# Kernel optimization log

Hardware: AMD Instinct MI355X
Metric: run time of the kernel (lower is better)

Reference implementation:

```python
import jax, jax.numpy as jnp
import numpy as np

# Detectron-style RPN GenerateProposals config (cfg[...].RPN_* in the original)
PRE_NMS_TOP_N = 6000
POST_NMS_TOP_N = 1000
NMS_THRESH = 0.7
MIN_SIZE = 16.0
FEAT_STRIDE = 16.0  # 1 / spatial_scale
BBOX_XFORM_CLIP = float(np.log(1000.0 / 16.0))


def _make_anchors():
    # 5 scales x 3 aspect ratios, centered at origin (Detectron-style)
    sizes = [32.0, 64.0, 128.0, 256.0, 512.0]
    ratios = [0.5, 1.0, 2.0]
    out = []
    for s in sizes:
        for r in ratios:
            w = s * np.sqrt(1.0 / r)
            h = s * np.sqrt(r)
            out.append([-(w - 1) / 2.0, -(h - 1) / 2.0, (w - 1) / 2.0, (h - 1) / 2.0])
    return np.asarray(out, dtype=np.float32)  # (15, 4)


def setup_inputs() -> dict:
    key = jax.random.key(0)
    k1, k2 = jax.random.split(key)
    N, A, H, W = 2, 15, 200, 200
    rpn_cls_prob = jax.random.uniform(k1, (N, A, H, W), dtype=jnp.float32)
    rpn_bbox_pred = jax.random.normal(k2, (N, 4 * A, H, W), dtype=jnp.float32) * 0.1
    im_h = H * FEAT_STRIDE
    im_w = W * FEAT_STRIDE
    im_info = jnp.tile(jnp.array([[im_h, im_w, 1.0]], dtype=jnp.float32), (N, 1))
    anchors = jnp.asarray(_make_anchors())
    return {"rpn_cls_prob": rpn_cls_prob, "rpn_bbox_pred": rpn_bbox_pred,
            "im_info": im_info, "anchors": anchors}


def _decode(anchors, deltas):
    # box_utils.bbox_transform with weights (1,1,1,1)
    ws = anchors[:, 2] - anchors[:, 0] + 1.0
    hs = anchors[:, 3] - anchors[:, 1] + 1.0
    cx = anchors[:, 0] + 0.5 * ws
    cy = anchors[:, 1] + 0.5 * hs
    dx, dy = deltas[:, 0], deltas[:, 1]
    dw = jnp.minimum(deltas[:, 2], BBOX_XFORM_CLIP)
    dh = jnp.minimum(deltas[:, 3], BBOX_XFORM_CLIP)
    pcx = dx * ws + cx
    pcy = dy * hs + cy
    pw = jnp.exp(dw) * ws
    ph = jnp.exp(dh) * hs
    return jnp.stack([pcx - 0.5 * pw, pcy - 0.5 * ph,
                      pcx + 0.5 * pw - 1.0, pcy + 0.5 * ph - 1.0], axis=1)


def _iou_matrix(boxes):
    # (P,4) -> (P,P), with +1 convention matching the original numpy code
    x1, y1, x2, y2 = boxes[:, 0], boxes[:, 1], boxes[:, 2], boxes[:, 3]
    areas = (x2 - x1 + 1.0) * (y2 - y1 + 1.0)
    xx1 = jnp.maximum(x1[:, None], x1[None, :])
    yy1 = jnp.maximum(y1[:, None], y1[None, :])
    xx2 = jnp.minimum(x2[:, None], x2[None, :])
    yy2 = jnp.minimum(y2[:, None], y2[None, :])
    iw = jnp.maximum(xx2 - xx1 + 1.0, 0.0)
    ih = jnp.maximum(yy2 - yy1 + 1.0, 0.0)
    inter = iw * ih
    return inter / (areas[:, None] + areas[None, :] - inter)


def _proposals_one_image(scores, deltas, im_info_i, all_anchors):
    # scores: (A,H,W); deltas: (4A,H,W); all_anchors: (K*A,4)
    P = PRE_NMS_TOP_N
    s = scores.transpose(1, 2, 0).reshape(-1)          # (K*A,)
    d = deltas.transpose(1, 2, 0).reshape(-1, 4)       # (K*A,4)
    vals, idx = jax.lax.top_k(s, P)                    # pre-NMS top-k
    props = _decode(all_anchors[idx], d[idx])          # (P,4)
    im_h, im_w, im_scale = im_info_i[0], im_info_i[1], im_info_i[2]
    # clip_tiled_boxes
    x1 = jnp.clip(props[:, 0], 0.0, im_w - 1.0)
    y1 = jnp.clip(props[:, 1], 0.0, im_h - 1.0)
    x2 = jnp.clip(props[:, 2], 0.0, im_w - 1.0)
    y2 = jnp.clip(props[:, 3], 0.0, im_h - 1.0)
    props = jnp.stack([x1, y1, x2, y2], axis=1)
    # _filter_boxes: mask out instead of removing (static shapes)
    min_size = MIN_SIZE * im_scale
    ws = x2 - x1 + 1.0
    hs = y2 - y1 + 1.0
    xc = x1 + ws / 2.0
    yc = y1 + hs / 2.0
    valid = (ws >= min_size) & (hs >= min_size) & (xc < im_w) & (yc < im_h)
    sc = jnp.where(valid, vals, -jnp.inf)
    order = jnp.argsort(-sc)                           # valid boxes first, by score
    props = props[order]
    sc = sc[order]
    valid = valid[order]
    # greedy NMS on score-sorted boxes
    iou = jax.lax.stop_gradient(_iou_matrix(props))    # (P,P)
    pos = jnp.arange(P)

    def step(keep, i):
        sup = (iou[i] > NMS_THRESH) & (pos > i) & keep[i]
        return keep & ~sup, None

    keep, _ = jax.lax.scan(step, valid, jnp.arange(P))
    final_sc = jnp.where(keep, sc, -jnp.inf)
    top_vals, top_idx = jax.lax.top_k(final_sc, POST_NMS_TOP_N)
    ok = jnp.isfinite(top_vals)
    out_props = jnp.where(ok[:, None], props[top_idx], 0.0)
    out_sc = jnp.where(ok, top_vals, 0.0)
    return out_props, out_sc


def reference(rpn_cls_prob, rpn_bbox_pred, im_info, anchors):
    N, A, H, W = rpn_cls_prob.shape
    # anchor shifting: all_anchors (K*A, 4)
    shift_x = jnp.arange(W, dtype=jnp.float32) * FEAT_STRIDE
    shift_y = jnp.arange(H, dtype=jnp.float32) * FEAT_STRIDE
    sx, sy = jnp.meshgrid(shift_x, shift_y)            # 'xy', matches np.meshgrid
    shifts = jnp.stack([sx.ravel(), sy.ravel(), sx.ravel(), sy.ravel()], axis=1)
    all_anchors = (anchors[None, :, :] + shifts[:, None, :]).reshape(-1, 4)
    props, sc = jax.vmap(
        lambda s, d, ii: _proposals_one_image(s, d, ii, all_anchors)
    )(rpn_cls_prob, rpn_bbox_pred, im_info)            # (N,R,4), (N,R)
    R = POST_NMS_TOP_N
    batch_inds = jnp.broadcast_to(
        jnp.arange(N, dtype=jnp.float32)[:, None, None], (N, R, 1))
    rois = jnp.concatenate([batch_inds, props], axis=2).reshape(N * R, 5)
    roi_probs = sc.reshape(N * R, 1)
    # pack [batch_ind, x1, y1, x2, y2, score] into one fixed-shape array
    return jnp.concatenate([rois, roi_probs], axis=1)  # (N*R, 6)
```

## Files before the change

kernel.cpp:

```cpp
#include <hip/hip_runtime.h>
#include <stdint.h>

#define N_IMG 2
#define A_NUM 15
#define HH 200
#define WW 200
#define HW 40000
#define K_TOT 600000
#define K_TOT4 150000
#define P_PRE 6000
#define R_POST 1000
#define NMS_T 0.7f
#define MIN_SZ 16.0f
#define FSTRIDE 16.0f
#define BBOX_CLIP 4.135166556742356f
#define CAND_CAP 8192
#define NWORDS 94
#define BINS 4096
#define MASK_BLOCKS 600
#define ZERO_WORDS (N_IMG * BINS * 2 + N_IMG * 16)
#define MID_T 0.7000000178813934326171875

typedef unsigned long long u64;
typedef uint32_t u32;

__device__ __forceinline__ u32 fkey(float s) {
    return __float_as_uint(s) | 0x80000000u;
}

__device__ __forceinline__ bool iou_gt(float ar, float arj,
                                       const float4& bi, const float4& bj) {
    float xx1 = fmaxf(bi.x, bj.x);
    float yy1 = fmaxf(bi.y, bj.y);
    float xx2 = fminf(bi.z, bj.z);
    float yy2 = fminf(bi.w, bj.w);
    float iw = fmaxf(xx2 - xx1 + 1.0f, 0.0f);
    float ih = fmaxf(yy2 - yy1 + 1.0f, 0.0f);
    float inter = iw * ih;
    float uni = (ar + arj) - inter;
    return (double)inter >= MID_T * (double)uni;
}

__global__ void k_zero(u32* __restrict__ w) {
    int i = blockIdx.x * 1024 + threadIdx.x;
    if (i < ZERO_WORDS) w[i] = 0u;
}

__global__ void k_histA(const float* __restrict__ sc, u32* __restrict__ histA,
                        u32* __restrict__ meta) {
    int n = blockIdx.y;
    __shared__ u32 h[BINS];
    __shared__ u32 part[256];
    __shared__ u32 isLast;
    for (int i = threadIdx.x; i < BINS; i += 256) h[i] = 0;
    __syncthreads();
    const float4* s4 = (const float4*)(sc + (size_t)n * K_TOT);
    for (int i = blockIdx.x * 256 + threadIdx.x; i < K_TOT4; i += 64 * 256) {
        float4 v = s4[i];
        atomicAdd(&h[fkey(v.x) >> 20], 1u);
        atomicAdd(&h[fkey(v.y) >> 20], 1u);
        atomicAdd(&h[fkey(v.z) >> 20], 1u);
        atomicAdd(&h[fkey(v.w) >> 20], 1u);
    }
    __syncthreads();
    for (int i = threadIdx.x; i < BINS; i += 256) {
        u32 v = h[i];
        if (v) atomicAdd(&histA[n * BINS + i], v);
    }
    __threadfence();
    if (threadIdx.x == 0)
        isLast = (atomicAdd(&meta[6], 1u) == (u32)(64 * N_IMG - 1)) ? 1u : 0u;
    __syncthreads();
    if (!isLast) return;
    for (int im = 0; im < N_IMG; ++im) {
        u32* hh = histA + im * BINS;
        u32 s = 0;
        for (int b = threadIdx.x * 16; b < threadIdx.x * 16 + 16; ++b)
            s += atomicAdd(&hh[b], 0u);
        part[threadIdx.x] = s;
        __syncthreads();
        if (threadIdx.x == 0) {
            u32 cum = 0; int seg = 255;
            for (; seg > 0; --seg) {
                if (cum + part[seg] >= P_PRE) break;
                cum += part[seg];
            }
            u32 cgt = cum; int bA = seg * 16; u32 hbA = 0;
            for (int b = seg * 16 + 15; b >= seg * 16; --b) {
                u32 hb = atomicAdd(&hh[b], 0u);
                if (cgt + hb >= P_PRE) { bA = b; hbA = hb; break; }
                cgt += hb;
            }
            meta[im * 16 + 0] = (u32)bA;
            meta[im * 16 + 1] = cgt;
            if (cgt + hbA <= CAND_CAP) {
                meta[im * 16 + 2] = ((u32)bA) << 12;
                meta[im * 16 + 8] = 0u;
            } else {
                meta[im * 16 + 8] = 1u;
            }
        }
        __syncthreads();
    }
}

__global__ void k_histB(const float* __restrict__ sc, u32* __restrict__ histB,
                        u32* __restrict__ meta) {
    int n = blockIdx.y;
    if (meta[n * 16 + 8] == 0u) return;
    __shared__ u32 h[BINS];
    __shared__ u32 part[256];
    __shared__ u32 isLast;
    for (int i = threadIdx.x; i < BINS; i += 256) h[i] = 0;
    __syncthreads();
    u32 bA = meta[n * 16 + 0];
    const float4* s4 = (const float4*)(sc + (size_t)n * K_TOT);
    for (int i = blockIdx.x * 256 + threadIdx.x; i < K_TOT4; i += 64 * 256) {
        float4 v = s4[i];
        u32 k0 = fkey(v.x), k1 = fkey(v.y), k2 = fkey(v.z), k3 = fkey(v.w);
        if ((k0 >> 20) == bA) atomicAdd(&h[(k0 >> 8) & 0xFFFu], 1u);
        if ((k1 >> 20) == bA) atomicAdd(&h[(k1 >> 8) & 0xFFFu], 1u);
        if ((k2 >> 20) == bA) atomicAdd(&h[(k2 >> 8) & 0xFFFu], 1u);
        if ((k3 >> 20) == bA) atomicAdd(&h[(k3 >> 8) & 0xFFFu], 1u);
    }
    __syncthreads();
    for (int i = threadIdx.x; i < BINS; i += 256) {
        u32 v = h[i];
        if (v) atomicAdd(&histB[n * BINS + i], v);
    }
    __threadfence();
    if (threadIdx.x == 0)
        isLast = (atomicAdd(&meta[n * 16 + 7], 1u) == 63u) ? 1u : 0u;
    __syncthreads();
    if (!isLast) return;
    {
        int im = n;
        u32* hh = histB + im * BINS;
        u32 s = 0;
        for (int b = threadIdx.x * 16; b < threadIdx.x * 16 + 16; ++b)
            s += atomicAdd(&hh[b], 0u);
        part[threadIdx.x] = s;
        __syncthreads();
        if (threadIdx.x == 0) {
            u32 cum = meta[im * 16 + 1];
            int seg = 255;
            for (; seg > 0; --seg) {
                if (cum + part[seg] >= P_PRE) break;
                cum += part[seg];
            }
            int bB = seg * 16;
            for (int b = seg * 16 + 15; b >= seg * 16; --b) {
                u32 hb = atomicAdd(&hh[b], 0u);
                if (cum + hb >= P_PRE) { bB = b; break; }
                cum += hb;
            }
            meta[im * 16 + 2] = (meta[im * 16 + 0] << 12) | (u32)bB;
        }
    }
}

__global__ void __launch_bounds__(256) k_compact(const float* __restrict__ sc,
                                                 u32* __restrict__ meta,
                                                 u64* __restrict__ cand) {
    int n = blockIdx.y;
    int tid = threadIdx.x;
    int lane = tid & 63, w = tid >> 6;
    int i4 = blockIdx.x * 256 + tid;
    u32 thr = meta[n * 16 + 2];
    float vv[4] = {0.f, 0.f, 0.f, 0.f};
    u32 flags = 0;
    if (i4 < K_TOT4) {
        const float4* s4 = (const float4*)(sc + (size_t)n * K_TOT);
        float4 v = s4[i4];
        vv[0] = v.x; vv[1] = v.y; vv[2] = v.z; vv[3] = v.w;
        #pragma unroll
        for (int e = 0; e < 4; ++e)
            if ((fkey(vv[e]) >> 8) >= thr) flags |= 1u << e;
    }
    u32 cnt = (u32)__popc(flags);
    u32 incl = cnt;
    #pragma unroll
    for (int off = 1; off < 64; off <<= 1) {
        u32 v = __shfl_up(incl, (unsigned)off);
        if (lane >= off) incl += v;
    }
    __shared__ u32 wtot[4];
    __shared__ u32 baseS;
    if (lane == 63) wtot[w] = incl;
    __syncthreads();
    if (tid == 0) {
        u32 tot = wtot[0] + wtot[1] + wtot[2] + wtot[3];
        baseS = atomicAdd(&meta[n * 16 + 3], tot);
    }
    __syncthreads();
    if (!flags) return;
    u32 wbase = 0;
    for (int i = 0; i < w; ++i) wbase += wtot[i];
    u32 pos = baseS + wbase + (incl - cnt);
    #pragma unroll
    for (int e = 0; e < 4; ++e) {
        if ((flags >> e) & 1u) {
            if (pos < CAND_CAP) {
                int el = i4 * 4 + e;
                int a = el / HW;
                int r = el - a * HW;
                u32 idx = (u32)(r * A_NUM + a);
                cand[n * CAND_CAP + pos] = ((u64)fkey(vv[e]) << 32) | (u32)(~idx);
            }
            pos++;
        }
    }
}

__global__ void __launch_bounds__(256) k_rankdec(
        const u64* __restrict__ cand, const u32* __restrict__ meta,
        const float* __restrict__ bbox, const float* __restrict__ iminfo,
        const float* __restrict__ anchors,
        float* __restrict__ topk_sc, float4* __restrict__ bbox4,
        u32* __restrict__ bval) {
    int n = blockIdx.y;
    u32 cnt = meta[n * 16 + 3];
    if (cnt > CAND_CAP) cnt = CAND_CAP;
    int base = blockIdx.x * 64;
    if (base >= (int)cnt) return;
    __shared__ u64 sk[CAND_CAP];
    __shared__ u32 pr[4][64];
    int tid = threadIdx.x, lane = tid & 63, w = tid >> 6;
    int cntPad = (int)((cnt + 7u) & ~7u);
    const u64* cn = cand + (size_t)n * CAND_CAP;
    for (int i = tid; i < cntPad; i += 256)
        sk[i] = (i < (int)cnt) ? cn[i] : 0ull;
    __syncthreads();
    int myi = base + lane;
    u64 mykey = (myi < (int)cnt) ? sk[myi] : 0ull;
    int stride = ((cntPad >> 2) + 7) & ~7;
    int j0 = w * stride;
    int j1 = min(j0 + stride, cntPad);
    int rank = 0;
    for (int j = j0; j < j1; j += 8) {
        u64 k0 = sk[j + 0], k1 = sk[j + 1], k2 = sk[j + 2], k3 = sk[j + 3];
        u64 k4 = sk[j + 4], k5 = sk[j + 5], k6 = sk[j + 6], k7 = sk[j + 7];
        rank += (int)(k0 > mykey) + (int)(k1 > mykey)
              + (int)(k2 > mykey) + (int)(k3 > mykey)
              + (int)(k4 > mykey) + (int)(k5 > mykey)
              + (int)(k6 > mykey) + (int)(k7 > mykey);
    }
    pr[w][lane] = (u32)rank;
    __syncthreads();
    if (w != 0 || myi >= (int)cnt) return;
    int r = (int)(pr[0][lane] + pr[1][lane] + pr[2][lane] + pr[3][lane]);
    if (r >= P_PRE) return;
    u32 idx = ~(u32)(mykey & 0xFFFFFFFFull);
    float score = __uint_as_float((u32)(mykey >> 32) ^ 0x80000000u);
    topk_sc[n * P_PRE + r] = score;
    int a = (int)(idx % A_NUM);
    int cell = (int)(idx / A_NUM);
    int ww = cell % WW, hh = cell / WW;
    float ax1 = anchors[a * 4 + 0] + FSTRIDE * (float)ww;
    float ay1 = anchors[a * 4 + 1] + FSTRIDE * (float)hh;
    float ax2 = anchors[a * 4 + 2] + FSTRIDE * (float)ww;
    float ay2 = anchors[a * 4 + 3] + FSTRIDE * (float)hh;
    float ws = ax2 - ax1 + 1.0f;
    float hs = ay2 - ay1 + 1.0f;
    float cx = ax1 + 0.5f * ws;
    float cy = ay1 + 0.5f * hs;
    const float* bb = bbox + (size_t)n * 4 * A_NUM * HW + hh * WW + ww;
    float dx = bb[(4 * a + 0) * HW];
    float dy = bb[(4 * a + 1) * HW];
    float dw = fminf(bb[(4 * a + 2) * HW], BBOX_CLIP);
    float dh = fminf(bb[(4 * a + 3) * HW], BBOX_CLIP);
    float pcx = dx * ws + cx, pcy = dy * hs + cy;
    float pw = expf(dw) * ws, ph = expf(dh) * hs;
    float x1 = pcx - 0.5f * pw;
    float y1 = pcy - 0.5f * ph;
    float x2 = pcx + 0.5f * pw - 1.0f;
    float y2 = pcy + 0.5f * ph - 1.0f;
    float im_h = iminfo[n * 3 + 0], im_w = iminfo[n * 3 + 1], iscale = iminfo[n * 3 + 2];
    x1 = fminf(fmaxf(x1, 0.0f), im_w - 1.0f);
    y1 = fminf(fmaxf(y1, 0.0f), im_h - 1.0f);
    x2 = fminf(fmaxf(x2, 0.0f), im_w - 1.0f);
    y2 = fminf(fmaxf(y2, 0.0f), im_h - 1.0f);
    float wss = x2 - x1 + 1.0f, hss = y2 - y1 + 1.0f;
    float xc = x1 + wss * 0.5f, yc = y1 + hss * 0.5f;
    float ms = MIN_SZ * iscale;
    bool valid = (wss >= ms) && (hss >= ms) && (xc < im_w) && (yc < im_h);
    float4 b; b.x = x1; b.y = y1; b.z = x2; b.w = y2;
    bbox4[n * P_PRE + r] = b;
    bval[n * P_PRE + r] = valid ? 1u : 0u;
}

__global__ void __launch_bounds__(1024) k_partition(
        const float4* __restrict__ bbox4,
        const float* __restrict__ bsc, const u32* __restrict__ bval,
        float4* __restrict__ sbox, float* __restrict__ ssc,
        float* __restrict__ sarea, u32* __restrict__ meta) {
    int n = blockIdx.x;
    int t = threadIdx.x;
    int lane = t & 63, w = t >> 6;
    int base = t * 6;
    u32 cnt = 0;
    if (base < P_PRE)
        for (int e = 0; e < 6; ++e) cnt += bval[n * P_PRE + base + e];
    u32 incl = cnt;
    #pragma unroll
    for (int off = 1; off < 64; off <<= 1) {
        u32 v = __shfl_up(incl, (unsigned)off);
        if (lane >= off) incl += v;
    }
    __shared__ u32 wtot[16];
    if (lane == 63) wtot[w] = incl;
    __syncthreads();
    u32 nv = 0, wbase = 0;
    #pragma unroll
    for (int i = 0; i < 16; ++i) {
        u32 x = wtot[i];
        if (i < w) wbase += x;
        nv += x;
    }
    u32 excl = wbase + (incl - cnt);
    if (t == 0) meta[n * 16 + 4] = nv;
    if (base < P_PRE) {
        u32 vseen = excl;
        for (int e = 0; e < 6; ++e) {
            int g = base + e;
            int src = n * P_PRE + g;
            u32 dst;
            if (bval[src]) { dst = vseen; vseen++; }
            else { dst = nv + (u32)g - vseen; }
            int d = n * P_PRE + (int)dst;
            float4 b = bbox4[src];
            sbox[d] = b;
            ssc[d] = bsc[src];
            sarea[d] = (b.z - b.x + 1.0f) * (b.w - b.y + 1.0f);
        }
    }
}

__global__ void __launch_bounds__(256) k_mask(const float4* __restrict__ sbox,
                                              const float* __restrict__ sarea,
                                              u64* __restrict__ mask,
                                              u64* __restrict__ selfmask) {
    int n = blockIdx.y;
    int rem = blockIdx.x;
    int ci = 0;
    while (true) {
        int g = (NWORDS - ci + 7) >> 3;
        if (rem < g) break;
        rem -= g;
        ++ci;
    }
    int cjBase = ci + (rem << 3);
    int lane = threadIdx.x & 63;
    int wv = threadIdx.x >> 6;
    __shared__ float4 sbi[64];
    __shared__ float sar[64];
    const float4* pb = sbox + n * P_PRE;
    const float* pa = sarea + n * P_PRE;
    if (threadIdx.x < 64) {
        int ic = min(ci * 64 + (int)threadIdx.x, P_PRE - 1);
        sbi[threadIdx.x] = pb[ic];
        sar[threadIdx.x] = pa[ic];
    }
    __syncthreads();
    #pragma unroll
    for (int sub = 0; sub < 2; ++sub) {
        int cj = cjBase + wv + sub * 4;
        if (cj >= NWORDS) continue;
        int j = cj * 64 + lane;
        int jc = min(j, P_PRE - 1);
        float4 bj = pb[jc];
        float arj = pa[jc];
        if (cj == ci) {
            u64 sm = 0;
            #pragma unroll 8
            for (int r = 0; r < 64; ++r) {
                bool sup = iou_gt(sar[r], arj, sbi[r], bj) && (r < lane);
                sm |= ((u64)sup) << r;
            }
            if (j < P_PRE) selfmask[(size_t)n * P_PRE + j] = sm;
        } else {
            u64 myword = 0;
            #pragma unroll 8
            for (int r = 0; r < 64; ++r) {
                u64 wrd = __ballot(iou_gt(sar[r], arj, sbi[r], bj));
                if (lane == r) myword = wrd;
            }
            int i = ci * 64 + lane;
            if (i < P_PRE)
                mask[((size_t)n * P_PRE + i) * NWORDS + cj] = myword;
        }
    }
}

__global__ void __launch_bounds__(1024) k_scan(
        const u64* __restrict__ mask, const u64* __restrict__ selfmask,
        const float4* __restrict__ sbox, const float* __restrict__ ssc,
        const u32* __restrict__ meta, float* __restrict__ out) {
    int n = blockIdx.x;
    int tid = threadIdx.x;
    int lane = tid & 63;
    int wv = tid >> 6;
    __shared__ u64 rem[NWORDS];
    __shared__ u64 smb[2][64];
    __shared__ u64 sA;
    __shared__ u32 rowsS[64];
    __shared__ int nkS;
    __shared__ u32 kidx[R_POST];
    __shared__ int keptS;
    u32 nv = meta[n * 16 + 4];
    const u64* mrow = mask + (size_t)n * P_PRE * NWORDS;
    const u64* smk = selfmask + (size_t)n * P_PRE;
    for (int c = tid; c < NWORDS; c += 1024) {
        int b0 = c * 64;
        rem[c] = ((u32)b0 >= nv) ? ~0ull
               : (((u32)(nv - b0) >= 64u) ? 0ull : ((~0ull) << (nv - b0)));
    }
    if (wv == 1) smb[0][lane] = smk[lane];
    if (tid == 0) keptS = 0;
    __syncthreads();
    for (int c = 0; c < NWORDS; ++c) {
        if (wv == 1 && (c + 1) < NWORDS) {
            int j = (c + 1) * 64 + lane;
            smb[(c + 1) & 1][lane] = (j < P_PRE) ? smk[j] : 0ull;
        }
        if (wv == 0) {
            u64 A = ~rem[c];
            if (A) {
                u64 sm = smb[c & 1][lane];
                u64 below = (1ull << lane) - 1ull;
                bool cand = ((A >> lane) & 1ull) != 0ull;
                while (true) {
                    bool sup = (sm & A & below) != 0ull;
                    u64 nA = __ballot(cand && !sup);
                    if (nA == A) break;
                    A = nA;
                }
                int kept = keptS;
                if ((A >> lane) & 1ull) {
                    int rk = (int)__popcll(A & below);
                    int pos = kept + rk;
                    if (pos < R_POST) kidx[pos] = (u32)(c * 64 + lane);
                    rowsS[rk] = (u32)lane;
                }
                if (lane == 0) {
                    keptS = kept + (int)__popcll(A);
                    nkS = (int)__popcll(A);
                    sA = A;
                }
            } else if (lane == 0) { sA = 0; nkS = 0; }
        }
        __syncthreads();
        if (keptS >= R_POST) break;
        if (sA) {
            int colSlot = tid & 127;
            int rg = tid >> 7;
            int col = c + 1 + colSlot;
            int nk = nkS;
            if (col < NWORDS && rg < nk) {
                int jbase = c * 64;
                u64 acc = 0;
                for (int r = rg; r < nk; r += 32) {
                    int r1 = r + 8, r2 = r + 16, r3 = r + 24;
                    u64 v0 = mrow[(size_t)(jbase + (int)rowsS[r]) * NWORDS + col];
                    u64 v1 = (r1 < nk) ? mrow[(size_t)(jbase + (int)rowsS[r1]) * NWORDS + col] : 0ull;
                    u64 v2 = (r2 < nk) ? mrow[(size_t)(jbase + (int)rowsS[r2]) * NWORDS + col] : 0ull;
                    u64 v3 = (r3 < nk) ? mrow[(size_t)(jbase + (int)rowsS[r3]) * NWORDS + col] : 0ull;
                    acc |= v0 | v1 | v2 | v3;
                }
                if (acc) atomicOr(&rem[col], acc);
            }
        }
        __syncthreads();
    }
    __syncthreads();
    int kept = keptS;
    for (int r = tid; r < R_POST; r += 1024) {
        float4 b = make_float4(0.f, 0.f, 0.f, 0.f);
        float s = 0.f;
        if (r < kept) {
            u32 i = kidx[r];
            b = sbox[n * P_PRE + (int)i];
            s = ssc[n * P_PRE + (int)i];
        }
        float* o = out + (size_t)(n * R_POST + r) * 6;
        o[0] = (float)n;
        o[1] = b.x; o[2] = b.y; o[3] = b.z; o[4] = b.w; o[5] = s;
    }
}

extern "C" void kernel_launch(void* const* d_in, const int* in_sizes, int n_in,
                              void* d_out, int out_size, void* d_ws, size_t ws_size,
                              hipStream_t stream) {
    const float* scores  = (const float*)d_in[0];
    const float* bbox    = (const float*)d_in[1];
    const float* iminfo  = (const float*)d_in[2];
    const float* anchors = (const float*)d_in[3];
    float* out = (float*)d_out;

    char* ws = (char*)d_ws;
    size_t off = 0;
    u32* histA = (u32*)(ws + off); off += (size_t)N_IMG * BINS * 4;
    u32* histB = (u32*)(ws + off); off += (size_t)N_IMG * BINS * 4;
    u32* meta  = (u32*)(ws + off); off += (size_t)N_IMG * 16 * 4;
    u64* cand      = (u64*)(ws + off);   off += (size_t)N_IMG * CAND_CAP * 8;
    float* topk_sc = (float*)(ws + off); off += (size_t)N_IMG * P_PRE * 4;
    float4* bbox4 = (float4*)(ws + off); off += (size_t)N_IMG * P_PRE * 16;
    u32* bval  = (u32*)(ws + off);       off += (size_t)N_IMG * P_PRE * 4;
    float4* sbox = (float4*)(ws + off);  off += (size_t)N_IMG * P_PRE * 16;
    float* ssc = (float*)(ws + off);     off += (size_t)N_IMG * P_PRE * 4;
    float* sarea = (float*)(ws + off);   off += (size_t)N_IMG * P_PRE * 4;
    u64* selfmask = (u64*)(ws + off);    off += (size_t)N_IMG * P_PRE * 8;
    u64* mask = (u64*)(ws + off);        off += (size_t)N_IMG * P_PRE * NWORDS * 8;
    (void)ws_size; (void)in_sizes; (void)n_in; (void)out_size;

    k_zero<<<(ZERO_WORDS + 1023) / 1024, 1024, 0, stream>>>((u32*)d_ws);

    dim3 gHist(64, N_IMG);
    k_histA<<<gHist, 256, 0, stream>>>(scores, histA, meta);
    k_histB<<<gHist, 256, 0, stream>>>(scores, histB, meta);
    dim3 gComp((K_TOT4 + 255) / 256, N_IMG);
    k_compact<<<gComp, 256, 0, stream>>>(scores, meta, cand);
    dim3 gRank(CAND_CAP / 64, N_IMG);
    k_rankdec<<<gRank, 256, 0, stream>>>(cand, meta, bbox, iminfo, anchors,
                                         topk_sc, bbox4, bval);
    k_partition<<<N_IMG, 1024, 0, stream>>>(bbox4, topk_sc, bval, sbox, ssc, sarea, meta);
    dim3 gMask(MASK_BLOCKS, N_IMG);
    k_mask<<<gMask, 256, 0, stream>>>(sbox, sarea, mask, selfmask);
    k_scan<<<N_IMG, 1024, 0, stream>>>(mask, selfmask, sbox, ssc, meta, out);
}
```

Baseline: 164.4 us.

## Fuse front-end top-k stages into one cooperative kernel with grid syncs

Replaces the zero, two histogram, compaction and rank/decode kernels with a single cooperative kernel of 128 blocks. Stages are separated by grid.sync instead of separate launches and last-block atomics. This removes several launch gaps. In exchange, compaction and rank/decode now run on only 128 blocks in loops instead of ~1200 and 256 blocks, which reduces parallelism.

```diff
diff --git a/kernel.cpp b/kernel.cpp
--- a/kernel.cpp
+++ b/kernel.cpp
@@ -1,5 +1,8 @@
 #include <hip/hip_runtime.h>
+#include <hip/hip_cooperative_groups.h>
 #include <stdint.h>
+
+namespace cg = cooperative_groups;
 
 #define N_IMG 2
 #define A_NUM 15
@@ -41,21 +44,35 @@
     return (double)inter >= MID_T * (double)uni;
 }
 
-__global__ void k_zero(u32* __restrict__ w) {
-    int i = blockIdx.x * 1024 + threadIdx.x;
-    if (i < ZERO_WORDS) w[i] = 0u;
-}
-
-__global__ void k_histA(const float* __restrict__ sc, u32* __restrict__ histA,
-                        u32* __restrict__ meta) {
-    int n = blockIdx.y;
-    __shared__ u32 h[BINS];
-    __shared__ u32 part[256];
-    __shared__ u32 isLast;
-    for (int i = threadIdx.x; i < BINS; i += 256) h[i] = 0;
+__global__ void __launch_bounds__(256) k_front(
+        const float* __restrict__ sc, const float* __restrict__ bbox,
+        const float* __restrict__ iminfo, const float* __restrict__ anchors,
+        u32* __restrict__ histA, u32* __restrict__ histB, u32* __restrict__ meta,
+        u64* __restrict__ cand, float* __restrict__ topk_sc,
+        float4* __restrict__ bbox4, u32* __restrict__ bval) {
+    cg::grid_group grid = cg::this_grid();
+    __shared__ u64 sk[CAND_CAP];
+    u32* h     = (u32*)sk;
+    u32* part  = (u32*)sk + BINS;
+    u32* wtot  = (u32*)sk + BINS + 256;
+    u32* baseS = (u32*)sk + BINS + 260;
+    u32* pr    = (u32*)sk + 16000;
+    int bid = blockIdx.x;
+    int tid = threadIdx.x;
+    int lane = tid & 63, w = tid >> 6;
+    int n = bid >> 6;
+    int bl = bid & 63;
+    const float4* s4 = (const float4*)(sc + (size_t)n * K_TOT);
+
+    {
+        int i = bid * 256 + tid;
+        if (i < ZERO_WORDS) histA[i] = 0u;
+    }
+    grid.sync();
+
+    for (int i = tid; i < BINS; i += 256) h[i] = 0;
     __syncthreads();
-    const float4* s4 = (const float4*)(sc + (size_t)n * K_TOT);
-    for (int i = blockIdx.x * 256 + threadIdx.x; i < K_TOT4; i += 64 * 256) {
+    for (int i = bl * 256 + tid; i < K_TOT4; i += 64 * 256) {
         float4 v = s4[i];
         atomicAdd(&h[fkey(v.x) >> 20], 1u);
         atomicAdd(&h[fkey(v.y) >> 20], 1u);
@@ -63,230 +80,222 @@
         atomicAdd(&h[fkey(v.w) >> 20], 1u);
     }
     __syncthreads();
-    for (int i = threadIdx.x; i < BINS; i += 256) {
+    for (int i = tid; i < BINS; i += 256) {
         u32 v = h[i];
         if (v) atomicAdd(&histA[n * BINS + i], v);
     }
-    __threadfence();
-    if (threadIdx.x == 0)
-        isLast = (atomicAdd(&meta[6], 1u) == (u32)(64 * N_IMG - 1)) ? 1u : 0u;
-    __syncthreads();
-    if (!isLast) return;
-    for (int im = 0; im < N_IMG; ++im) {
-        u32* hh = histA + im * BINS;
-        u32 s = 0;
-        for (int b = threadIdx.x * 16; b < threadIdx.x * 16 + 16; ++b)
-            s += atomicAdd(&hh[b], 0u);
-        part[threadIdx.x] = s;
-        __syncthreads();
-        if (threadIdx.x == 0) {
-            u32 cum = 0; int seg = 255;
-            for (; seg > 0; --seg) {
-                if (cum + part[seg] >= P_PRE) break;
-                cum += part[seg];
-            }
-            u32 cgt = cum; int bA = seg * 16; u32 hbA = 0;
-            for (int b = seg * 16 + 15; b >= seg * 16; --b) {
-                u32 hb = atomicAdd(&hh[b], 0u);
-                if (cgt + hb >= P_PRE) { bA = b; hbA = hb; break; }
-                cgt += hb;
-            }
-            meta[im * 16 + 0] = (u32)bA;
-            meta[im * 16 + 1] = cgt;
-            if (cgt + hbA <= CAND_CAP) {
-                meta[im * 16 + 2] = ((u32)bA) << 12;
-                meta[im * 16 + 8] = 0u;
-            } else {
-                meta[im * 16 + 8] = 1u;
-            }
-        }
-        __syncthreads();
-    }
-}
-
-__global__ void k_histB(const float* __restrict__ sc, u32* __restrict__ histB,
-                        u32* __restrict__ meta) {
-    int n = blockIdx.y;
-    if (meta[n * 16 + 8] == 0u) return;
-    __shared__ u32 h[BINS];
-    __shared__ u32 part[256];
-    __shared__ u32 isLast;
-    for (int i = threadIdx.x; i < BINS; i += 256) h[i] = 0;
-    __syncthreads();
-    u32 bA = meta[n * 16 + 0];
-    const float4* s4 = (const float4*)(sc + (size_t)n * K_TOT);
-    for (int i = blockIdx.x * 256 + threadIdx.x; i < K_TOT4; i += 64 * 256) {
-        float4 v = s4[i];
-        u32 k0 = fkey(v.x), k1 = fkey(v.y), k2 = fkey(v.z), k3 = fkey(v.w);
-        if ((k0 >> 20) == bA) atomicAdd(&h[(k0 >> 8) & 0xFFFu], 1u);
-        if ((k1 >> 20) == bA) atomicAdd(&h[(k1 >> 8) & 0xFFFu], 1u);
-        if ((k2 >> 20) == bA) atomicAdd(&h[(k2 >> 8) & 0xFFFu], 1u);
-        if ((k3 >> 20) == bA) atomicAdd(&h[(k3 >> 8) & 0xFFFu], 1u);
-    }
-    __syncthreads();
-    for (int i = threadIdx.x; i < BINS; i += 256) {
-        u32 v = h[i];
-        if (v) atomicAdd(&histB[n * BINS + i], v);
-    }
-    __threadfence();
-    if (threadIdx.x == 0)
-        isLast = (atomicAdd(&meta[n * 16 + 7], 1u) == 63u) ? 1u : 0u;
-    __syncthreads();
-    if (!isLast) return;
+    grid.sync();
+
+    if (bid == 0) {
+        for (int im = 0; im < N_IMG; ++im) {
+            u32* hh = histA + im * BINS;
+            u32 s = 0;
+            for (int b = tid * 16; b < tid * 16 + 16; ++b) s += hh[b];
+            part[tid] = s;
+            __syncthreads();
+            if (tid == 0) {
+                u32 cum = 0; int seg = 255;
+                for (; seg > 0; --seg) {
+                    if (cum + part[seg] >= P_PRE) break;
+                    cum += part[seg];
+                }
+                u32 cgt = cum; int bA = seg * 16; u32 hbA = 0;
+                for (int b = seg * 16 + 15; b >= seg * 16; --b) {
+                    u32 hb = hh[b];
+                    if (cgt + hb >= P_PRE) { bA = b; hbA = hb; break; }
+                    cgt += hb;
+                }
+                meta[im * 16 + 0] = (u32)bA;
+                meta[im * 16 + 1] = cgt;
+                if (cgt + hbA <= CAND_CAP) {
+                    meta[im * 16 + 2] = ((u32)bA) << 12;
+                    meta[im * 16 + 8] = 0u;
+                } else {
+                    meta[im * 16 + 8] = 1u;
+                }
+            }
+            __syncthreads();
+        }
+    }
+    grid.sync();
+
+    bool needB = (meta[8] != 0u) || (meta[16 + 8] != 0u);
+    if (needB) {
+        bool mine = meta[n * 16 + 8] != 0u;
+        for (int i = tid; i < BINS; i += 256) h[i] = 0;
+        __syncthreads();
+        if (mine) {
+            u32 bA = meta[n * 16 + 0];
+            for (int i = bl * 256 + tid; i < K_TOT4; i += 64 * 256) {
+                float4 v = s4[i];
+                u32 k0 = fkey(v.x), k1 = fkey(v.y), k2 = fkey(v.z), k3 = fkey(v.w);
+                if ((k0 >> 20) == bA) atomicAdd(&h[(k0 >> 8) & 0xFFFu], 1u);
+                if ((k1 >> 20) == bA) atomicAdd(&h[(k1 >> 8) & 0xFFFu], 1u);
+                if ((k2 >> 20) == bA) atomicAdd(&h[(k2 >> 8) & 0xFFFu], 1u);
+                if ((k3 >> 20) == bA) atomicAdd(&h[(k3 >> 8) & 0xFFFu], 1u);
+            }
+        }
+        __syncthreads();
+        if (mine)
+            for (int i = tid; i < BINS; i += 256) {
+                u32 v = h[i];
+                if (v) atomicAdd(&histB[n * BINS + i], v);
+            }
+        grid.sync();
+        if (bid == 0) {
+            for (int im = 0; im < N_IMG; ++im) {
+                if (meta[im * 16 + 8] == 0u) continue;
+                u32* hh = histB + im * BINS;
+                u32 s = 0;
+                for (int b = tid * 16; b < tid * 16 + 16; ++b) s += hh[b];
+                part[tid] = s;
+                __syncthreads();
+                if (tid == 0) {
+                    u32 cum = meta[im * 16 + 1];
+                    int seg = 255;
+                    for (; seg > 0; --seg) {
+                        if (cum + part[seg] >= P_PRE) break;
+                        cum += part[seg];
+                    }
+                    int bB = seg * 16;
+                    for (int b = seg * 16 + 15; b >= seg * 16; --b) {
+                        u32 hb = hh[b];
+                        if (cum + hb >= P_PRE) { bB = b; break; }
+                        cum += hb;
+                    }
+                    meta[im * 16 + 2] = (meta[im * 16 + 0] << 12) | (u32)bB;
+                }
+                __syncthreads();
+            }
+        }
+        grid.sync();
+    }
+
     {
-        int im = n;
-        u32* hh = histB + im * BINS;
-        u32 s = 0;
-        for (int b = threadIdx.x * 16; b < threadIdx.x * 16 + 16; ++b)
-            s += atomicAdd(&hh[b], 0u);
-        part[threadIdx.x] = s;
-        __syncthreads();
-        if (threadIdx.x == 0) {
-            u32 cum = meta[im * 16 + 1];
-            int seg = 255;
-            for (; seg > 0; --seg) {
-                if (cum + part[seg] >= P_PRE) break;
-                cum += part[seg];
-            }
-            int bB = seg * 16;
-            for (int b = seg * 16 + 15; b >= seg * 16; --b) {
-                u32 hb = atomicAdd(&hh[b], 0u);
-                if (cum + hb >= P_PRE) { bB = b; break; }
-                cum += hb;
-            }
-            meta[im * 16 + 2] = (meta[im * 16 + 0] << 12) | (u32)bB;
-        }
-    }
-}
-
-__global__ void __launch_bounds__(256) k_compact(const float* __restrict__ sc,
-                                                 u32* __restrict__ meta,
-                                                 u64* __restrict__ cand) {
-    int n = blockIdx.y;
-    int tid = threadIdx.x;
-    int lane = tid & 63, w = tid >> 6;
-    int i4 = blockIdx.x * 256 + tid;
-    u32 thr = meta[n * 16 + 2];
-    float vv[4] = {0.f, 0.f, 0.f, 0.f};
-    u32 flags = 0;
-    if (i4 < K_TOT4) {
-        const float4* s4 = (const float4*)(sc + (size_t)n * K_TOT);
-        float4 v = s4[i4];
-        vv[0] = v.x; vv[1] = v.y; vv[2] = v.z; vv[3] = v.w;
-        #pragma unroll
-        for (int e = 0; e < 4; ++e)
-            if ((fkey(vv[e]) >> 8) >= thr) flags |= 1u << e;
-    }
-    u32 cnt = (u32)__popc(flags);
-    u32 incl = cnt;
-    #pragma unroll
-    for (int off = 1; off < 64; off <<= 1) {
-        u32 v = __shfl_up(incl, (unsigned)off);
-        if (lane >= off) incl += v;
-    }
-    __shared__ u32 wtot[4];
-    __shared__ u32 baseS;
-    if (lane == 63) wtot[w] = incl;
-    __syncthreads();
-    if (tid == 0) {
-        u32 tot = wtot[0] + wtot[1] + wtot[2] + wtot[3];
-        baseS = atomicAdd(&meta[n * 16 + 3], tot);
-    }
-    __syncthreads();
-    if (!flags) return;
-    u32 wbase = 0;
-    for (int i = 0; i < w; ++i) wbase += wtot[i];
-    u32 pos = baseS + wbase + (incl - cnt);
-    #pragma unroll
-    for (int e = 0; e < 4; ++e) {
-        if ((flags >> e) & 1u) {
-            if (pos < CAND_CAP) {
-                int el = i4 * 4 + e;
-                int a = el / HW;
-                int r = el - a * HW;
-                u32 idx = (u32)(r * A_NUM + a);
-                cand[n * CAND_CAP + pos] = ((u64)fkey(vv[e]) << 32) | (u32)(~idx);
-            }
-            pos++;
-        }
-    }
-}
-
-__global__ void __launch_bounds__(256) k_rankdec(
-        const u64* __restrict__ cand, const u32* __restrict__ meta,
-        const float* __restrict__ bbox, const float* __restrict__ iminfo,
-        const float* __restrict__ anchors,
-        float* __restrict__ topk_sc, float4* __restrict__ bbox4,
-        u32* __restrict__ bval) {
-    int n = blockIdx.y;
-    u32 cnt = meta[n * 16 + 3];
-    if (cnt > CAND_CAP) cnt = CAND_CAP;
-    int base = blockIdx.x * 64;
-    if (base >= (int)cnt) return;
-    __shared__ u64 sk[CAND_CAP];
-    __shared__ u32 pr[4][64];
-    int tid = threadIdx.x, lane = tid & 63, w = tid >> 6;
-    int cntPad = (int)((cnt + 7u) & ~7u);
-    const u64* cn = cand + (size_t)n * CAND_CAP;
-    for (int i = tid; i < cntPad; i += 256)
-        sk[i] = (i < (int)cnt) ? cn[i] : 0ull;
-    __syncthreads();
-    int myi = base + lane;
-    u64 mykey = (myi < (int)cnt) ? sk[myi] : 0ull;
-    int stride = ((cntPad >> 2) + 7) & ~7;
-    int j0 = w * stride;
-    int j1 = min(j0 + stride, cntPad);
-    int rank = 0;
-    for (int j = j0; j < j1; j += 8) {
-        u64 k0 = sk[j + 0], k1 = sk[j + 1], k2 = sk[j + 2], k3 = sk[j + 3];
-        u64 k4 = sk[j + 4], k5 = sk[j + 5], k6 = sk[j + 6], k7 = sk[j + 7];
-        rank += (int)(k0 > mykey) + (int)(k1 > mykey)
-              + (int)(k2 > mykey) + (int)(k3 > mykey)
-              + (int)(k4 > mykey) + (int)(k5 > mykey)
-              + (int)(k6 > mykey) + (int)(k7 > mykey);
-    }
-    pr[w][lane] = (u32)rank;
-    __syncthreads();
-    if (w != 0 || myi >= (int)cnt) return;
-    int r = (int)(pr[0][lane] + pr[1][lane] + pr[2][lane] + pr[3][lane]);
-    if (r >= P_PRE) return;
-    u32 idx = ~(u32)(mykey & 0xFFFFFFFFull);
-    float score = __uint_as_float((u32)(mykey >> 32) ^ 0x80000000u);
-    topk_sc[n * P_PRE + r] = score;
-    int a = (int)(idx % A_NUM);
-    int cell = (int)(idx / A_NUM);
-    int ww = cell % WW, hh = cell / WW;
-    float ax1 = anchors[a * 4 + 0] + FSTRIDE * (float)ww;
-    float ay1 = anchors[a * 4 + 1] + FSTRIDE * (float)hh;
-    float ax2 = anchors[a * 4 + 2] + FSTRIDE * (float)ww;
-    float ay2 = anchors[a * 4 + 3] + FSTRIDE * (float)hh;
-    float ws = ax2 - ax1 + 1.0f;
-    float hs = ay2 - ay1 + 1.0f;
-    float cx = ax1 + 0.5f * ws;
-    float cy = ay1 + 0.5f * hs;
-    const float* bb = bbox + (size_t)n * 4 * A_NUM * HW + hh * WW + ww;
-    float dx = bb[(4 * a + 0) * HW];
-    float dy = bb[(4 * a + 1) * HW];
-    float dw = fminf(bb[(4 * a + 2) * HW], BBOX_CLIP);
-    float dh = fminf(bb[(4 * a + 3) * HW], BBOX_CLIP);
-    float pcx = dx * ws + cx, pcy = dy * hs + cy;
-    float pw = expf(dw) * ws, ph = expf(dh) * hs;
-    float x1 = pcx - 0.5f * pw;
-    float y1 = pcy - 0.5f * ph;
-    float x2 = pcx + 0.5f * pw - 1.0f;
-    float y2 = pcy + 0.5f * ph - 1.0f;
-    float im_h = iminfo[n * 3 + 0], im_w = iminfo[n * 3 + 1], iscale = iminfo[n * 3 + 2];
-    x1 = fminf(fmaxf(x1, 0.0f), im_w - 1.0f);
-    y1 = fminf(fmaxf(y1, 0.0f), im_h - 1.0f);
-    x2 = fminf(fmaxf(x2, 0.0f), im_w - 1.0f);
-    y2 = fminf(fmaxf(y2, 0.0f), im_h - 1.0f);
-    float wss = x2 - x1 + 1.0f, hss = y2 - y1 + 1.0f;
-    float xc = x1 + wss * 0.5f, yc = y1 + hss * 0.5f;
-    float ms = MIN_SZ * iscale;
-    bool valid = (wss >= ms) && (hss >= ms) && (xc < im_w) && (yc < im_h);
-    float4 b; b.x = x1; b.y = y1; b.z = x2; b.w = y2;
-    bbox4[n * P_PRE + r] = b;
-    bval[n * P_PRE + r] = valid ? 1u : 0u;
+        u32 thr = meta[n * 16 + 2];
+        const int ITERS = (K_TOT4 + 64 * 256 - 1) / (64 * 256);
+        for (int it = 0; it < ITERS; ++it) {
+            int i4 = it * (64 * 256) + bl * 256 + tid;
+            float vv[4] = {0.f, 0.f, 0.f, 0.f};
+            u32 flags = 0;
+            if (i4 < K_TOT4) {
+                float4 v = s4[i4];
+                vv[0] = v.x; vv[1] = v.y; vv[2] = v.z; vv[3] = v.w;
+                #pragma unroll
+                for (int e = 0; e < 4; ++e)
+                    if ((fkey(vv[e]) >> 8) >= thr) flags |= 1u << e;
+            }
+            u32 cnt = (u32)__popc(flags);
+            u32 incl = cnt;
+            #pragma unroll
+            for (int off = 1; off < 64; off <<= 1) {
+                u32 v = __shfl_up(incl, (unsigned)off);
+                if (lane >= off) incl += v;
+            }
+            if (lane == 63) wtot[w] = incl;
+            __syncthreads();
+            if (tid == 0) {
+                u32 tot = wtot[0] + wtot[1] + wtot[2] + wtot[3];
+                *baseS = atomicAdd(&meta[n * 16 + 3], tot);
+            }
+            __syncthreads();
+            if (flags) {
+                u32 wbase = 0;
+                for (int i = 0; i < w; ++i) wbase += wtot[i];
+                u32 pos = *baseS + wbase + (incl - cnt);
+                #pragma unroll
+                for (int e = 0; e < 4; ++e) {
+                    if ((flags >> e) & 1u) {
+                        if (pos < CAND_CAP) {
+                            int el = i4 * 4 + e;
+                            int a = el / HW;
+                            int r = el - a * HW;
+                            u32 idx = (u32)(r * A_NUM + a);
+                            cand[n * CAND_CAP + pos] = ((u64)fkey(vv[e]) << 32) | (u32)(~idx);
+                        }
+                        pos++;
+                    }
+                }
+            }
+            __syncthreads();
+        }
+    }
+    grid.sync();
+
+    for (int g = bid; g < 2 * (CAND_CAP / 64); g += 128) {
+        int n2 = g >> 7;
+        int base = (g & 127) * 64;
+        u32 cnt = meta[n2 * 16 + 3];
+        if (cnt > CAND_CAP) cnt = CAND_CAP;
+        if (base >= (int)cnt) continue;
+        int cntPad = (int)((cnt + 7u) & ~7u);
+        const u64* cn = cand + (size_t)n2 * CAND_CAP;
+        __syncthreads();
+        for (int i = tid; i < cntPad; i += 256)
+            sk[i] = (i < (int)cnt) ? cn[i] : 0ull;
+        __syncthreads();
+        int myi = base + lane;
+        u64 mykey = (myi < (int)cnt) ? sk[myi] : 0ull;
+        int stride = ((cntPad >> 2) + 7) & ~7;
+        int j0 = w * stride;
+        int j1 = min(j0 + stride, cntPad);
+        int rank = 0;
+        for (int j = j0; j < j1; j += 8) {
+            u64 k0 = sk[j + 0], k1 = sk[j + 1], k2 = sk[j + 2], k3 = sk[j + 3];
+            u64 k4 = sk[j + 4], k5 = sk[j + 5], k6 = sk[j + 6], k7 = sk[j + 7];
+            rank += (int)(k0 > mykey) + (int)(k1 > mykey)
+                  + (int)(k2 > mykey) + (int)(k3 > mykey)
+                  + (int)(k4 > mykey) + (int)(k5 > mykey)
+                  + (int)(k6 > mykey) + (int)(k7 > mykey);
+        }
+        pr[w * 64 + lane] = (u32)rank;
+        __syncthreads();
+        if (w == 0 && myi < (int)cnt) {
+            int r = (int)(pr[lane] + pr[64 + lane] + pr[128 + lane] + pr[192 + lane]);
+            if (r < P_PRE) {
+                u64 kk = mykey;
+                u32 idx = ~(u32)(kk & 0xFFFFFFFFull);
+                float score = __uint_as_float((u32)(kk >> 32) ^ 0x80000000u);
+                topk_sc[n2 * P_PRE + r] = score;
+                int a = (int)(idx % A_NUM);
+                int cell = (int)(idx / A_NUM);
+                int ww = cell % WW, hh = cell / WW;
+                float ax1 = anchors[a * 4 + 0] + FSTRIDE * (float)ww;
+                float ay1 = anchors[a * 4 + 1] + FSTRIDE * (float)hh;
+                float ax2 = anchors[a * 4 + 2] + FSTRIDE * (float)ww;
+                float ay2 = anchors[a * 4 + 3] + FSTRIDE * (float)hh;
+                float ws = ax2 - ax1 + 1.0f;
+                float hs = ay2 - ay1 + 1.0f;
+                float cx = ax1 + 0.5f * ws;
+                float cy = ay1 + 0.5f * hs;
+                const float* bb = bbox + (size_t)n2 * 4 * A_NUM * HW + hh * WW + ww;
+                float dx = bb[(4 * a + 0) * HW];
+                float dy = bb[(4 * a + 1) * HW];
+                float dw = fminf(bb[(4 * a + 2) * HW], BBOX_CLIP);
+                float dh = fminf(bb[(4 * a + 3) * HW], BBOX_CLIP);
+                float pcx = dx * ws + cx, pcy = dy * hs + cy;
+                float pw = expf(dw) * ws, ph = expf(dh) * hs;
+                float x1 = pcx - 0.5f * pw;
+                float y1 = pcy - 0.5f * ph;
+                float x2 = pcx + 0.5f * pw - 1.0f;
+                float y2 = pcy + 0.5f * ph - 1.0f;
+                float im_h = iminfo[n2 * 3 + 0], im_w = iminfo[n2 * 3 + 1];
+                float iscale = iminfo[n2 * 3 + 2];
+                x1 = fminf(fmaxf(x1, 0.0f), im_w - 1.0f);
+                y1 = fminf(fmaxf(y1, 0.0f), im_h - 1.0f);
+                x2 = fminf(fmaxf(x2, 0.0f), im_w - 1.0f);
+                y2 = fminf(fmaxf(y2, 0.0f), im_h - 1.0f);
+                float wss = x2 - x1 + 1.0f, hss = y2 - y1 + 1.0f;
+                float xc = x1 + wss * 0.5f, yc = y1 + hss * 0.5f;
+                float ms = MIN_SZ * iscale;
+                bool valid = (wss >= ms) && (hss >= ms) && (xc < im_w) && (yc < im_h);
+                float4 b; b.x = x1; b.y = y1; b.z = x2; b.w = y2;
+                bbox4[n2 * P_PRE + r] = b;
+                bval[n2 * P_PRE + r] = valid ? 1u : 0u;
+            }
+        }
+        __syncthreads();
+    }
 }
 
 __global__ void __launch_bounds__(1024) k_partition(
@@ -513,16 +522,11 @@
     u64* mask = (u64*)(ws + off);        off += (size_t)N_IMG * P_PRE * NWORDS * 8;
     (void)ws_size; (void)in_sizes; (void)n_in; (void)out_size;
 
-    k_zero<<<(ZERO_WORDS + 1023) / 1024, 1024, 0, stream>>>((u32*)d_ws);
-
-    dim3 gHist(64, N_IMG);
-    k_histA<<<gHist, 256, 0, stream>>>(scores, histA, meta);
-    k_histB<<<gHist, 256, 0, stream>>>(scores, histB, meta);
-    dim3 gComp((K_TOT4 + 255) / 256, N_IMG);
-    k_compact<<<gComp, 256, 0, stream>>>(scores, meta, cand);
-    dim3 gRank(CAND_CAP / 64, N_IMG);
-    k_rankdec<<<gRank, 256, 0, stream>>>(cand, meta, bbox, iminfo, anchors,
-                                         topk_sc, bbox4, bval);
+    void* args[] = {(void*)&scores, (void*)&bbox, (void*)&iminfo, (void*)&anchors,
+                    (void*)&histA, (void*)&histB, (void*)&meta, (void*)&cand,
+                    (void*)&topk_sc, (void*)&bbox4, (void*)&bval};
+    hipLaunchCooperativeKernel((void*)k_front, dim3(128), dim3(256), args, 0, stream);
+
     k_partition<<<N_IMG, 1024, 0, stream>>>(bbox4, topk_sc, bval, sbox, ssc, sarea, meta);
     dim3 gMask(MASK_BLOCKS, N_IMG);
     k_mask<<<gMask, 256, 0, stream>>>(sbox, sarea, mask, selfmask);
```

After: 252.5 us. 1.54x slower.
